# Kernel optimization log

Hardware: AMD Instinct MI355X
Metric: run time of the kernel (lower is better)

The kernel has to match this reference:

```python
import jax, jax.numpy as jnp
import numpy as np

LN_EPS = 1e-5


def setup_inputs() -> dict:
    key = jax.random.key(0)
    ks = jax.random.split(key, 10)
    B, T, D, K = 32, 1024, 512, 3
    enc = jax.random.normal(ks[0], (B, T, D), jnp.float32)
    dur = jax.random.randint(ks[1], (B, T), 0, 7, jnp.int32)
    s = 0.02
    return {
        "encoder_output": enc,
        "duration_target": dur,
        "conv1_w": jax.random.normal(ks[2], (K, D, D), jnp.float32) * s,  # HIO layout
        "conv1_b": jnp.zeros((D,), jnp.float32),
        "ln1_w": jnp.ones((D,), jnp.float32),
        "ln1_b": jnp.zeros((D,), jnp.float32),
        "conv2_w": jax.random.normal(ks[3], (K, D, D), jnp.float32) * s,
        "conv2_b": jnp.zeros((D,), jnp.float32),
        "ln2_w": jnp.ones((D,), jnp.float32),
        "ln2_b": jnp.zeros((D,), jnp.float32),
        "lin_w": jax.random.normal(ks[4], (D, 1), jnp.float32) * s,
        "lin_b": jnp.zeros((1,), jnp.float32),
        "max_len": 4096,
    }


def _conv_relu(x, w, b):
    # x: [B,T,D], w: [K, D_in, D_out] ('HIO'), 'SAME' padding == torch padding=1 for k=3
    y = jax.lax.conv_general_dilated(
        x, w, window_strides=(1,), padding="SAME",
        dimension_numbers=("NHC", "HIO", "NHC"))
    return jax.nn.relu(y + b)


def _layernorm(x, g, b):
    mu = jnp.mean(x, axis=-1, keepdims=True)
    var = jnp.mean(jnp.square(x - mu), axis=-1, keepdims=True)
    return (x - mu) * jax.lax.rsqrt(var + LN_EPS) * g + b


def reference(encoder_output, duration_target, conv1_w, conv1_b, ln1_w, ln1_b,
              conv2_w, conv2_b, ln2_w, ln2_b, lin_w, lin_b, max_len):
    B, T, D = encoder_output.shape
    # duration predictor: conv -> relu -> LN -> conv -> relu -> LN -> linear
    h = _layernorm(_conv_relu(encoder_output, conv1_w, conv1_b), ln1_w, ln1_b)
    h = _layernorm(_conv_relu(h, conv2_w, conv2_b), ln2_w, ln2_b)
    duration_predictor_output = (h @ lin_w + lin_b)[..., 0]  # [B,T]

    # training path: expand by duration_target via fused gather with cumulative offsets
    cum = jnp.cumsum(duration_target, axis=1)          # [B,T]
    pos = jnp.arange(max_len, dtype=jnp.int32)         # [L]
    # src index for output frame j: first t with cum[t] > j
    idx = jax.vmap(lambda c: jnp.searchsorted(c, pos, side="right"))(cum)  # [B,L]
    valid = pos[None, :] < cum[:, -1:]                  # [B,L]
    idx = jnp.minimum(idx, T - 1)
    expanded = jnp.take_along_axis(encoder_output, idx[:, :, None], axis=1)
    expanded = expanded * valid[:, :, None].astype(encoder_output.dtype)
    return expanded, duration_predictor_output
```

## Files before the change

kernel.cpp:

```cpp
#include <hip/hip_runtime.h>
#include <hip/hip_bf16.h>

#define BB 32
#define TT 1024
#define DD 512
#define LL 4096
#define KDIM 1536
#define TP 1026
#define ROWS (BB * TT)
#define NT (KDIM / 32)

typedef __attribute__((ext_vector_type(8))) short short8;
typedef __attribute__((ext_vector_type(8))) unsigned short ushort8;
typedef __attribute__((ext_vector_type(4))) float floatx4;

__device__ __forceinline__ unsigned short f2bf(float f) {
  unsigned int u = __builtin_bit_cast(unsigned int, f);
  u += 0x7FFF + ((u >> 16) & 1);
  return (unsigned short)(u >> 16);
}
__device__ __forceinline__ float bf2f(unsigned short h) {
  return __builtin_bit_cast(float, (unsigned int)h << 16);
}

#define GLOAD_LDS16(g, l)                                          \
  __builtin_amdgcn_global_load_lds(                                \
      (const __attribute__((address_space(1))) void*)(g),          \
      (__attribute__((address_space(3))) void*)(l), 16, 0, 0)

#define PAD_BLKS ((BB * TP) / 4)
#define W0 (PAD_BLKS + 16)
#define C0 (W0 + 384)
#define PREP_BLKS (C0 + 32)

__global__ __launch_bounds__(256) void prep_kernel(
    const float* __restrict__ X, unsigned short* __restrict__ Xp,
    unsigned short* __restrict__ Hp,
    const float* __restrict__ W1, unsigned short* __restrict__ Wt1,
    const float* __restrict__ W2, unsigned short* __restrict__ Wt2,
    const int* __restrict__ dur, int* __restrict__ cum) {
  __shared__ float tile[64][65];
  const int tid = threadIdx.x;
  const int lane = tid & 63;

  if (blockIdx.x >= C0) {
    int* ls = reinterpret_cast<int*>(tile);
    const int b = blockIdx.x - C0;
    int4 v = reinterpret_cast<const int4*>(dur + b * TT)[tid];
    const int s0 = v.x, s1 = s0 + v.y, s2 = s1 + v.z, s3 = s2 + v.w;
    ls[tid] = s3;
    __syncthreads();
    for (int off = 1; off < 256; off <<= 1) {
      int x = (tid >= off) ? ls[tid - off] : 0;
      __syncthreads();
      ls[tid] += x;
      __syncthreads();
    }
    const int base = tid ? ls[tid - 1] : 0;
    int4 o = {base + s0, base + s1, base + s2, base + s3};
    reinterpret_cast<int4*>(cum + b * TT)[tid] = o;
    return;
  }
  if (blockIdx.x >= W0) {
    const int w = blockIdx.x - W0;
    const int z = w / 192;
    const int rem = w - z * 192;
    const int bx = rem & 7;
    const int by = rem >> 3;
    const float* W = z ? W2 : W1;
    unsigned short* Wt = z ? Wt2 : Wt1;
    const int n0 = bx * 64;
    const int k0 = by * 64;
    const int c = lane;
    const int r4 = tid >> 6;
#pragma unroll
    for (int r = 0; r < 16; ++r)
      tile[r * 4 + r4][c] = W[(long)(k0 + r * 4 + r4) * DD + n0 + c];
    __syncthreads();
#pragma unroll
    for (int r = 0; r < 16; ++r)
      Wt[(long)(n0 + r * 4 + r4) * KDIM + k0 + c] = f2bf(tile[c][r * 4 + r4]);
    return;
  }
  if (blockIdx.x >= PAD_BLKS) {
    const int hid = (blockIdx.x - PAD_BLKS) * 4 + (tid >> 6);
    const int b = hid >> 1;
    const long r = (long)b * TP + ((hid & 1) ? (TP - 1) : 0);
    *reinterpret_cast<ushort8*>(Hp + r * DD + lane * 8) = (ushort8)0;
    return;
  }
  const int row = blockIdx.x * 4 + (tid >> 6);
  const int b  = row / TP;
  const int pr = row - b * TP;
  ushort8* o = reinterpret_cast<ushort8*>(Xp + (long)row * DD + lane * 8);
  ushort8 v;
  if (pr == 0 || pr == TP - 1) {
    v = (ushort8)0;
  } else {
    const float* p = X + ((long)(b * TT + pr - 1)) * DD + lane * 8;
    float4 a = *reinterpret_cast<const float4*>(p);
    float4 c = *reinterpret_cast<const float4*>(p + 4);
    v[0] = f2bf(a.x); v[1] = f2bf(a.y); v[2] = f2bf(a.z); v[3] = f2bf(a.w);
    v[4] = f2bf(c.x); v[5] = f2bf(c.y); v[6] = f2bf(c.z); v[7] = f2bf(c.w);
  }
  *o = v;
}

template <int LAYER>
__global__ __launch_bounds__(512, 2) void fused_conv_ln_kernel(
    const unsigned short* __restrict__ Xp, const unsigned short* __restrict__ Wt,
    const float* __restrict__ bias, const float* __restrict__ g,
    const float* __restrict__ be, const float* __restrict__ lw,
    const float* __restrict__ lb, unsigned short* __restrict__ Hp,
    float* __restrict__ dpo) {
  __shared__ unsigned short As[3][128 * 32];
  __shared__ unsigned short Bs[3][512 * 32];
  __shared__ float sS[4][128];
  __shared__ float sQ[4][128];
  __shared__ float muL[128];
  __shared__ float rsL[128];

  const int tid  = threadIdx.x;
  const int lane = tid & 63;
  const int wid  = tid >> 6;
  const int srow = lane >> 2;
  const int gchunk = (lane & 3) ^ (srow & 3);
  const int frow = lane & 15;
  const int quad = lane >> 4;
  const int rdch = quad ^ (frow & 3);
  const int wm = (wid >> 2) * 64;
  const int wn = (wid & 3) * 128;
  const int wc = wid & 3;

  const int m0 = blockIdx.x * 128;
  const int bA = m0 >> 10;
  const int t0 = m0 & (TT - 1);

  const unsigned short* gA0 =
      Xp + (long)(bA * TP + t0 + wid * 16 + srow) * DD + gchunk * 8;
  const unsigned short* gB0 =
      Wt + (long)(wid * 16 + srow) * KDIM + gchunk * 8;

  floatx4 acc[4][8];
#pragma unroll
  for (int i = 0; i < 4; ++i)
#pragma unroll
    for (int j = 0; j < 8; ++j) acc[i][j] = (floatx4){0.f, 0.f, 0.f, 0.f};

#define STAGE(bi, kk)                                                         \
  do {                                                                        \
    const int tap_ = (kk) >> 9;                                               \
    const int c0_  = (kk) & 511;                                              \
    GLOAD_LDS16(gA0 + (long)tap_ * DD + c0_, &As[bi][(wid * 16) * 32]);       \
    GLOAD_LDS16(gB0 + (kk),                   &Bs[bi][(wid * 16) * 32]);      \
    GLOAD_LDS16(gB0 + (long)128 * KDIM + (kk), &Bs[bi][(128 + wid * 16) * 32]); \
    GLOAD_LDS16(gB0 + (long)256 * KDIM + (kk), &Bs[bi][(256 + wid * 16) * 32]); \
    GLOAD_LDS16(gB0 + (long)384 * KDIM + (kk), &Bs[bi][(384 + wid * 16) * 32]); \
  } while (0)

#define COMPUTE(bi)                                                           \
  do {                                                                        \
    short8 a_[4], b_[8];                                                      \
    _Pragma("unroll")                                                         \
    for (int i = 0; i < 4; ++i)                                               \
      a_[i] = *reinterpret_cast<const short8*>(                               \
          &As[bi][(wm + i * 16 + frow) * 32 + rdch * 8]);                     \
    _Pragma("unroll")                                                         \
    for (int j = 0; j < 8; ++j)                                               \
      b_[j] = *reinterpret_cast<const short8*>(                               \
          &Bs[bi][(wn + j * 16 + frow) * 32 + rdch * 8]);                     \
    _Pragma("unroll")                                                         \
    for (int i = 0; i < 4; ++i)                                               \
      _Pragma("unroll")                                                       \
      for (int j = 0; j < 8; ++j)                                             \
        acc[i][j] = __builtin_amdgcn_mfma_f32_16x16x32_bf16(                  \
            a_[i], b_[j], acc[i][j], 0, 0, 0);                                \
  } while (0)

  STAGE(0, 0);
  STAGE(1, 32);

  int cur = 0;
  int stg = 2;
  for (int t = 0; t < NT - 1; ++t) {
    asm volatile("s_waitcnt vmcnt(5)" ::: "memory");
    __builtin_amdgcn_s_barrier();
    __builtin_amdgcn_sched_barrier(0);
    if (t + 2 < NT) STAGE(stg, (t + 2) * 32);
    COMPUTE(cur);
    cur = (cur == 2) ? 0 : cur + 1;
    stg = (stg == 2) ? 0 : stg + 1;
  }
  asm volatile("s_waitcnt vmcnt(0)" ::: "memory");
  __builtin_amdgcn_s_barrier();
  __builtin_amdgcn_sched_barrier(0);
  COMPUTE(cur);
#undef STAGE
#undef COMPUTE

  float bz[8];
#pragma unroll
  for (int j = 0; j < 8; ++j) bz[j] = bias[wn + j * 16 + frow];
#pragma unroll
  for (int i = 0; i < 4; ++i)
#pragma unroll
    for (int j = 0; j < 8; ++j)
#pragma unroll
      for (int r = 0; r < 4; ++r)
        acc[i][j][r] = fmaxf(acc[i][j][r] + bz[j], 0.f);

  float ps[16], pq[16];
#pragma unroll
  for (int i = 0; i < 4; ++i)
#pragma unroll
    for (int r = 0; r < 4; ++r) {
      float s = 0.f, q = 0.f;
#pragma unroll
      for (int j = 0; j < 8; ++j) {
        const float v = acc[i][j][r];
        s += v; q += v * v;
      }
      ps[i * 4 + r] = s; pq[i * 4 + r] = q;
    }
#pragma unroll
  for (int off = 1; off < 16; off <<= 1)
#pragma unroll
    for (int k = 0; k < 16; ++k) {
      ps[k] += __shfl_xor(ps[k], off);
      pq[k] += __shfl_xor(pq[k], off);
    }
  if (frow == 0) {
#pragma unroll
    for (int i = 0; i < 4; ++i)
#pragma unroll
      for (int r = 0; r < 4; ++r) {
        const int row = wm + i * 16 + quad * 4 + r;
        sS[wc][row] = ps[i * 4 + r];
        sQ[wc][row] = pq[i * 4 + r];
      }
  }
  __syncthreads();
  if (tid < 128) {
    const float s = sS[0][tid] + sS[1][tid] + sS[2][tid] + sS[3][tid];
    const float q = sQ[0][tid] + sQ[1][tid] + sQ[2][tid] + sQ[3][tid];
    const float mu = s * (1.f / DD);
    const float var = q * (1.f / DD) - mu * mu;
    muL[tid] = mu;
    rsL[tid] = rsqrtf(var + 1e-5f);
  }
  __syncthreads();

  float gg[8], bb[8];
#pragma unroll
  for (int j = 0; j < 8; ++j) {
    gg[j] = g[wn + j * 16 + frow];
    bb[j] = be[wn + j * 16 + frow];
  }

  if constexpr (LAYER == 1) {
    unsigned short* Ls = &Bs[0][0];
    const int h = wm >> 6;
#pragma unroll
    for (int ph = 0; ph < 2; ++ph) {
      __syncthreads();
      if (h == ph) {
#pragma unroll
        for (int i = 0; i < 4; ++i)
#pragma unroll
          for (int r = 0; r < 4; ++r) {
            const int row = wm + i * 16 + quad * 4 + r;
            const float mu = muL[row];
            const float rs = rsL[row];
            const int lrow = row - ph * 64;
#pragma unroll
            for (int j = 0; j < 8; ++j) {
              const float v = (acc[i][j][r] - mu) * rs * gg[j] + bb[j];
              Ls[lrow * 520 + wn + j * 16 + frow] = f2bf(v);
            }
          }
      }
      __syncthreads();
      const long gbase = (long)(bA * TP + t0 + ph * 64 + 1) * DD;
#pragma unroll
      for (int it = 0; it < 8; ++it) {
        const int r2 = it * 8 + wid;
        const int cc = lane * 8;
        ushort8 val = *reinterpret_cast<const ushort8*>(&Ls[r2 * 520 + cc]);
        *reinterpret_cast<ushort8*>(&Hp[gbase + (long)r2 * DD + cc]) = val;
      }
    }
  } else {
    float ww[8];
#pragma unroll
    for (int j = 0; j < 8; ++j) ww[j] = lw[wn + j * 16 + frow];
#pragma unroll
    for (int i = 0; i < 4; ++i)
#pragma unroll
      for (int r = 0; r < 4; ++r) {
        const int row = wm + i * 16 + quad * 4 + r;
        const float mu = muL[row];
        const float rs = rsL[row];
        float d = 0.f;
#pragma unroll
        for (int j = 0; j < 8; ++j) {
          const float v = (acc[i][j][r] - mu) * rs * gg[j] + bb[j];
          d += v * ww[j];
        }
#pragma unroll
        for (int off = 1; off < 16; off <<= 1) d += __shfl_xor(d, off);
        if (frow == 0) sS[wc][row] = d;
      }
    __syncthreads();
    if (tid < 128)
      dpo[m0 + tid] =
          sS[0][tid] + sS[1][tid] + sS[2][tid] + sS[3][tid] + lb[0];
  }
}

__global__ __launch_bounds__(512) void gather_kernel(
    const float* __restrict__ X, const int* __restrict__ cum,
    float* __restrict__ out) {
  const long gf = (long)blockIdx.x * 4 + (threadIdx.x >> 7);
  const int tl = threadIdx.x & 127;
  const int b = (int)(gf >> 12);
  const int j = (int)(gf & (LL - 1));
  const int* c = cum + b * TT;
  floatx4* o = reinterpret_cast<floatx4*>(out + gf * DD) + tl;
  const int total = c[TT - 1];
  if (j >= total) {
    __builtin_nontemporal_store((floatx4){0.f, 0.f, 0.f, 0.f}, o);
    return;
  }
  int lo = 0, hi = TT - 1;
  while (lo < hi) {
    const int mid = (lo + hi) >> 1;
    if (c[mid] <= j) lo = mid + 1; else hi = mid;
  }
  const floatx4* src =
      reinterpret_cast<const floatx4*>(X + ((long)b * TT + lo) * DD) + tl;
  __builtin_nontemporal_store(*src, o);
}

extern "C" void kernel_launch(void* const* d_in, const int* in_sizes, int n_in,
                              void* d_out, int out_size, void* d_ws,
                              size_t ws_size, hipStream_t stream) {
  const float* enc = (const float*)d_in[0];
  const int* dur   = (const int*)d_in[1];
  const float* w1  = (const float*)d_in[2];
  const float* b1  = (const float*)d_in[3];
  const float* g1  = (const float*)d_in[4];
  const float* be1 = (const float*)d_in[5];
  const float* w2  = (const float*)d_in[6];
  const float* b2  = (const float*)d_in[7];
  const float* g2  = (const float*)d_in[8];
  const float* be2 = (const float*)d_in[9];
  const float* lw  = (const float*)d_in[10];
  const float* lb  = (const float*)d_in[11];

  float* out = (float*)d_out;
  float* expanded = out;
  float* dpo = out + (long)BB * LL * DD;

  unsigned short* enc_pad = (unsigned short*)(expanded);
  unsigned short* h1_pad  = (unsigned short*)(expanded + 9000000);
  unsigned short* wt1     = (unsigned short*)(expanded + 18000000);
  unsigned short* wt2     = (unsigned short*)(expanded + 18400000);
  int* cum = (int*)d_ws;

  prep_kernel<<<PREP_BLKS, 256, 0, stream>>>(enc, enc_pad, h1_pad, w1, wt1,
                                             w2, wt2, dur, cum);

  fused_conv_ln_kernel<1><<<ROWS / 128, 512, 0, stream>>>(
      enc_pad, wt1, b1, g1, be1, nullptr, nullptr, h1_pad, nullptr);
  fused_conv_ln_kernel<2><<<ROWS / 128, 512, 0, stream>>>(
      h1_pad, wt2, b2, g2, be2, lw, lb, nullptr, dpo);

  gather_kernel<<<BB * LL / 4, 512, 0, stream>>>(enc, cum, expanded);
}
```

Measured before the change: 542.4 us.

## Use 1024-thread conv blocks, precompute gather indices, drop nontemporal stores

The fused conv+LayerNorm kernel now runs 16 waves per block, each owning a 64x64 output tile instead of 64x128. This halves the accumulator registers per wave and raises the number of waves per CU. Source frame indices are now written once in prep_kernel from the cumulative durations, replacing a per-frame binary search in the gather kernel. The gather's nontemporal stores become plain stores. Risks: more LDS traffic per MFMA from the smaller warp tiles, a serial per-thread fill loop in prep, and the 4-blocks-per-CU launch bound may not fit the shared-memory footprint.

```diff
diff --git a/kernel.cpp b/kernel.cpp
--- a/kernel.cpp
+++ b/kernel.cpp
@@ -19,9 +19,6 @@
   u += 0x7FFF + ((u >> 16) & 1);
   return (unsigned short)(u >> 16);
 }
-__device__ __forceinline__ float bf2f(unsigned short h) {
-  return __builtin_bit_cast(float, (unsigned int)h << 16);
-}
 
 #define GLOAD_LDS16(g, l)                                          \
   __builtin_amdgcn_global_load_lds(                                \
@@ -38,7 +35,8 @@
     unsigned short* __restrict__ Hp,
     const float* __restrict__ W1, unsigned short* __restrict__ Wt1,
     const float* __restrict__ W2, unsigned short* __restrict__ Wt2,
-    const int* __restrict__ dur, int* __restrict__ cum) {
+    const int* __restrict__ dur, int* __restrict__ cum,
+    int* __restrict__ idx) {
   __shared__ float tile[64][65];
   const int tid = threadIdx.x;
   const int lane = tid & 63;
@@ -59,6 +57,15 @@
     const int base = tid ? ls[tid - 1] : 0;
     int4 o = {base + s0, base + s1, base + s2, base + s3};
     reinterpret_cast<int4*>(cum + b * TT)[tid] = o;
+    int* ib = idx + b * LL;
+    int st = base;
+    const int dv[4] = {v.x, v.y, v.z, v.w};
+#pragma unroll
+    for (int k = 0; k < 4; ++k) {
+      const int e = min(st + dv[k], LL);
+      for (int j = st; j < e; ++j) ib[j] = 4 * tid + k;
+      st += dv[k];
+    }
     return;
   }
   if (blockIdx.x >= W0) {
@@ -107,7 +114,7 @@
 }
 
 template <int LAYER>
-__global__ __launch_bounds__(512, 2) void fused_conv_ln_kernel(
+__global__ __launch_bounds__(1024, 4) void fused_conv_ln_kernel(
     const unsigned short* __restrict__ Xp, const unsigned short* __restrict__ Wt,
     const float* __restrict__ bias, const float* __restrict__ g,
     const float* __restrict__ be, const float* __restrict__ lw,
@@ -115,8 +122,8 @@
     float* __restrict__ dpo) {
   __shared__ unsigned short As[3][128 * 32];
   __shared__ unsigned short Bs[3][512 * 32];
-  __shared__ float sS[4][128];
-  __shared__ float sQ[4][128];
+  __shared__ float sS[8][128];
+  __shared__ float sQ[8][128];
   __shared__ float muL[128];
   __shared__ float rsL[128];
 
@@ -128,51 +135,51 @@
   const int frow = lane & 15;
   const int quad = lane >> 4;
   const int rdch = quad ^ (frow & 3);
-  const int wm = (wid >> 2) * 64;
-  const int wn = (wid & 3) * 128;
-  const int wc = wid & 3;
+  const int wm = (wid >> 3) * 64;
+  const int wn = (wid & 7) * 64;
+  const int wc = wid & 7;
 
   const int m0 = blockIdx.x * 128;
   const int bA = m0 >> 10;
   const int t0 = m0 & (TT - 1);
 
   const unsigned short* gA0 =
-      Xp + (long)(bA * TP + t0 + wid * 16 + srow) * DD + gchunk * 8;
+      Xp + (long)(bA * TP + t0 + (wid & 7) * 16 + srow) * DD + gchunk * 8;
+  const int bb0 = (wid < 8) ? wid * 32 : 256 + (wid - 8) * 32;
   const unsigned short* gB0 =
-      Wt + (long)(wid * 16 + srow) * KDIM + gchunk * 8;
-
-  floatx4 acc[4][8];
+      Wt + (long)(bb0 + srow) * KDIM + gchunk * 8;
+
+  floatx4 acc[4][4];
 #pragma unroll
   for (int i = 0; i < 4; ++i)
 #pragma unroll
-    for (int j = 0; j < 8; ++j) acc[i][j] = (floatx4){0.f, 0.f, 0.f, 0.f};
+    for (int j = 0; j < 4; ++j) acc[i][j] = (floatx4){0.f, 0.f, 0.f, 0.f};
 
 #define STAGE(bi, kk)                                                         \
   do {                                                                        \
     const int tap_ = (kk) >> 9;                                               \
     const int c0_  = (kk) & 511;                                              \
-    GLOAD_LDS16(gA0 + (long)tap_ * DD + c0_, &As[bi][(wid * 16) * 32]);       \
-    GLOAD_LDS16(gB0 + (kk),                   &Bs[bi][(wid * 16) * 32]);      \
-    GLOAD_LDS16(gB0 + (long)128 * KDIM + (kk), &Bs[bi][(128 + wid * 16) * 32]); \
-    GLOAD_LDS16(gB0 + (long)256 * KDIM + (kk), &Bs[bi][(256 + wid * 16) * 32]); \
-    GLOAD_LDS16(gB0 + (long)384 * KDIM + (kk), &Bs[bi][(384 + wid * 16) * 32]); \
+    if (wid < 8)                                                              \
+      GLOAD_LDS16(gA0 + (long)tap_ * DD + c0_, &As[bi][(wid * 16) * 32]);     \
+    GLOAD_LDS16(gB0 + (kk),                &Bs[bi][bb0 * 32]);                \
+    GLOAD_LDS16(gB0 + (long)16 * KDIM + (kk), &Bs[bi][(bb0 + 16) * 32]);      \
   } while (0)
 
 #define COMPUTE(bi)                                                           \
   do {                                                                        \
-    short8 a_[4], b_[8];                                                      \
+    short8 a_[4], b_[4];                                                      \
     _Pragma("unroll")                                                         \
     for (int i = 0; i < 4; ++i)                                               \
       a_[i] = *reinterpret_cast<const short8*>(                               \
           &As[bi][(wm + i * 16 + frow) * 32 + rdch * 8]);                     \
     _Pragma("unroll")                                                         \
-    for (int j = 0; j < 8; ++j)                                               \
+    for (int j = 0; j < 4; ++j)                                               \
       b_[j] = *reinterpret_cast<const short8*>(                               \
           &Bs[bi][(wn + j * 16 + frow) * 32 + rdch * 8]);                     \
     _Pragma("unroll")                                                         \
     for (int i = 0; i < 4; ++i)                                               \
       _Pragma("unroll")                                                       \
-      for (int j = 0; j < 8; ++j)                                             \
+      for (int j = 0; j < 4; ++j)                                             \
         acc[i][j] = __builtin_amdgcn_mfma_f32_16x16x32_bf16(                  \
             a_[i], b_[j], acc[i][j], 0, 0, 0);                                \
   } while (0)
@@ -183,7 +190,8 @@
   int cur = 0;
   int stg = 2;
   for (int t = 0; t < NT - 1; ++t) {
-    asm volatile("s_waitcnt vmcnt(5)" ::: "memory");
+    if (wid < 8) asm volatile("s_waitcnt vmcnt(3)" ::: "memory");
+    else         asm volatile("s_waitcnt vmcnt(2)" ::: "memory");
     __builtin_amdgcn_s_barrier();
     __builtin_amdgcn_sched_barrier(0);
     if (t + 2 < NT) STAGE(stg, (t + 2) * 32);
@@ -198,13 +206,13 @@
 #undef STAGE
 #undef COMPUTE
 
-  float bz[8];
-#pragma unroll
-  for (int j = 0; j < 8; ++j) bz[j] = bias[wn + j * 16 + frow];
+  float bz[4];
+#pragma unroll
+  for (int j = 0; j < 4; ++j) bz[j] = bias[wn + j * 16 + frow];
 #pragma unroll
   for (int i = 0; i < 4; ++i)
 #pragma unroll
-    for (int j = 0; j < 8; ++j)
+    for (int j = 0; j < 4; ++j)
 #pragma unroll
       for (int r = 0; r < 4; ++r)
         acc[i][j][r] = fmaxf(acc[i][j][r] + bz[j], 0.f);
@@ -216,7 +224,7 @@
     for (int r = 0; r < 4; ++r) {
       float s = 0.f, q = 0.f;
 #pragma unroll
-      for (int j = 0; j < 8; ++j) {
+      for (int j = 0; j < 4; ++j) {
         const float v = acc[i][j][r];
         s += v; q += v * v;
       }
@@ -241,8 +249,9 @@
   }
   __syncthreads();
   if (tid < 128) {
-    const float s = sS[0][tid] + sS[1][tid] + sS[2][tid] + sS[3][tid];
-    const float q = sQ[0][tid] + sQ[1][tid] + sQ[2][tid] + sQ[3][tid];
+    float s = 0.f, q = 0.f;
+#pragma unroll
+    for (int c = 0; c < 8; ++c) { s += sS[c][tid]; q += sQ[c][tid]; }
     const float mu = s * (1.f / DD);
     const float var = q * (1.f / DD) - mu * mu;
     muL[tid] = mu;
@@ -250,9 +259,9 @@
   }
   __syncthreads();
 
-  float gg[8], bb[8];
-#pragma unroll
-  for (int j = 0; j < 8; ++j) {
+  float gg[4], bb[4];
+#pragma unroll
+  for (int j = 0; j < 4; ++j) {
     gg[j] = g[wn + j * 16 + frow];
     bb[j] = be[wn + j * 16 + frow];
   }
@@ -273,7 +282,7 @@
             const float rs = rsL[row];
             const int lrow = row - ph * 64;
 #pragma unroll
-            for (int j = 0; j < 8; ++j) {
+            for (int j = 0; j < 4; ++j) {
               const float v = (acc[i][j][r] - mu) * rs * gg[j] + bb[j];
               Ls[lrow * 520 + wn + j * 16 + frow] = f2bf(v);
             }
@@ -282,17 +291,17 @@
       __syncthreads();
       const long gbase = (long)(bA * TP + t0 + ph * 64 + 1) * DD;
 #pragma unroll
-      for (int it = 0; it < 8; ++it) {
-        const int r2 = it * 8 + wid;
+      for (int it = 0; it < 4; ++it) {
+        const int r2 = it * 16 + wid;
         const int cc = lane * 8;
         ushort8 val = *reinterpret_cast<const ushort8*>(&Ls[r2 * 520 + cc]);
         *reinterpret_cast<ushort8*>(&Hp[gbase + (long)r2 * DD + cc]) = val;
       }
     }
   } else {
-    float ww[8];
-#pragma unroll
-    for (int j = 0; j < 8; ++j) ww[j] = lw[wn + j * 16 + frow];
+    float ww[4];
+#pragma unroll
+    for (int j = 0; j < 4; ++j) ww[j] = lw[wn + j * 16 + frow];
 #pragma unroll
     for (int i = 0; i < 4; ++i)
 #pragma unroll
@@ -302,7 +311,7 @@
         const float rs = rsL[row];
         float d = 0.f;
 #pragma unroll
-        for (int j = 0; j < 8; ++j) {
+        for (int j = 0; j < 4; ++j) {
           const float v = (acc[i][j][r] - mu) * rs * gg[j] + bb[j];
           d += v * ww[j];
         }
@@ -311,34 +320,32 @@
         if (frow == 0) sS[wc][row] = d;
       }
     __syncthreads();
-    if (tid < 128)
-      dpo[m0 + tid] =
-          sS[0][tid] + sS[1][tid] + sS[2][tid] + sS[3][tid] + lb[0];
+    if (tid < 128) {
+      float s = lb[0];
+#pragma unroll
+      for (int c = 0; c < 8; ++c) s += sS[c][tid];
+      dpo[blockIdx.x * 128 + tid] = s;
+    }
   }
 }
 
 __global__ __launch_bounds__(512) void gather_kernel(
     const float* __restrict__ X, const int* __restrict__ cum,
-    float* __restrict__ out) {
+    const int* __restrict__ idx, float* __restrict__ out) {
   const long gf = (long)blockIdx.x * 4 + (threadIdx.x >> 7);
   const int tl = threadIdx.x & 127;
   const int b = (int)(gf >> 12);
   const int j = (int)(gf & (LL - 1));
-  const int* c = cum + b * TT;
+  const int total = cum[b * TT + TT - 1];
   floatx4* o = reinterpret_cast<floatx4*>(out + gf * DD) + tl;
-  const int total = c[TT - 1];
   if (j >= total) {
-    __builtin_nontemporal_store((floatx4){0.f, 0.f, 0.f, 0.f}, o);
+    *o = (floatx4){0.f, 0.f, 0.f, 0.f};
     return;
   }
-  int lo = 0, hi = TT - 1;
-  while (lo < hi) {
-    const int mid = (lo + hi) >> 1;
-    if (c[mid] <= j) lo = mid + 1; else hi = mid;
-  }
+  const int lo = idx[b * LL + j];
   const floatx4* src =
       reinterpret_cast<const floatx4*>(X + ((long)b * TT + lo) * DD) + tl;
-  __builtin_nontemporal_store(*src, o);
+  *o = *src;
 }
 
 extern "C" void kernel_launch(void* const* d_in, const int* in_sizes, int n_in,
@@ -366,14 +373,15 @@
   unsigned short* wt1     = (unsigned short*)(expanded + 18000000);
   unsigned short* wt2     = (unsigned short*)(expanded + 18400000);
   int* cum = (int*)d_ws;
+  int* idx = (int*)d_ws + ROWS;
 
   prep_kernel<<<PREP_BLKS, 256, 0, stream>>>(enc, enc_pad, h1_pad, w1, wt1,
-                                             w2, wt2, dur, cum);
-
-  fused_conv_ln_kernel<1><<<ROWS / 128, 512, 0, stream>>>(
+                                             w2, wt2, dur, cum, idx);
+
+  fused_conv_ln_kernel<1><<<ROWS / 128, 1024, 0, stream>>>(
       enc_pad, wt1, b1, g1, be1, nullptr, nullptr, h1_pad, nullptr);
-  fused_conv_ln_kernel<2><<<ROWS / 128, 512, 0, stream>>>(
+  fused_conv_ln_kernel<2><<<ROWS / 128, 1024, 0, stream>>>(
       h1_pad, wt2, b2, g2, be2, lw, lb, nullptr, dpo);
 
-  gather_kernel<<<BB * LL / 4, 512, 0, stream>>>(enc, cum, expanded);
-}
+  gather_kernel<<<BB * LL / 4, 512, 0, stream>>>(enc, cum, idx, expanded);
+}
```

Measured after the change: 513.7 us. 5.3% less time.

## Split MFMA step into halves, widen LDS swizzle, precompute gather indices

Applied to the files above, without the earlier changes.

The GEMM main loop now loads B fragments in two halves. Each half is followed by an explicit lgkmcnt wait, and the MFMA blocks run at raised priority with a barrier between them, which interleaves LDS reads with matrix math. The LDS XOR swizzle gains an extra term to reduce bank conflicts. The prep kernel now writes a per-frame source index table, so the gather kernel replaces its per-thread binary search with one lookup. The gather also switches from nontemporal stores to plain stores. Building the index table with serial per-thread loops adds some prep time and workspace use.

```diff
diff --git a/kernel.cpp b/kernel.cpp
--- a/kernel.cpp
+++ b/kernel.cpp
@@ -19,9 +19,6 @@
   u += 0x7FFF + ((u >> 16) & 1);
   return (unsigned short)(u >> 16);
 }
-__device__ __forceinline__ float bf2f(unsigned short h) {
-  return __builtin_bit_cast(float, (unsigned int)h << 16);
-}
 
 #define GLOAD_LDS16(g, l)                                          \
   __builtin_amdgcn_global_load_lds(                                \
@@ -38,7 +35,8 @@
     unsigned short* __restrict__ Hp,
     const float* __restrict__ W1, unsigned short* __restrict__ Wt1,
     const float* __restrict__ W2, unsigned short* __restrict__ Wt2,
-    const int* __restrict__ dur, int* __restrict__ cum) {
+    const int* __restrict__ dur, int* __restrict__ cum,
+    int* __restrict__ idx) {
   __shared__ float tile[64][65];
   const int tid = threadIdx.x;
   const int lane = tid & 63;
@@ -59,6 +57,15 @@
     const int base = tid ? ls[tid - 1] : 0;
     int4 o = {base + s0, base + s1, base + s2, base + s3};
     reinterpret_cast<int4*>(cum + b * TT)[tid] = o;
+    int* ib = idx + b * LL;
+    int st = base;
+    const int dv[4] = {v.x, v.y, v.z, v.w};
+#pragma unroll
+    for (int k = 0; k < 4; ++k) {
+      const int e = min(st + dv[k], LL);
+      for (int j = st; j < e; ++j) ib[j] = 4 * tid + k;
+      st += dv[k];
+    }
     return;
   }
   if (blockIdx.x >= W0) {
@@ -124,10 +131,10 @@
   const int lane = tid & 63;
   const int wid  = tid >> 6;
   const int srow = lane >> 2;
-  const int gchunk = (lane & 3) ^ (srow & 3);
+  const int gchunk = (lane & 3) ^ (srow & 3) ^ ((srow >> 2) & 3);
   const int frow = lane & 15;
   const int quad = lane >> 4;
-  const int rdch = quad ^ (frow & 3);
+  const int rdch = quad ^ (frow & 3) ^ ((frow >> 2) & 3);
   const int wm = (wid >> 2) * 64;
   const int wn = (wid & 3) * 128;
   const int wc = wid & 3;
@@ -158,23 +165,45 @@
     GLOAD_LDS16(gB0 + (long)384 * KDIM + (kk), &Bs[bi][(384 + wid * 16) * 32]); \
   } while (0)
 
-#define COMPUTE(bi)                                                           \
+#define STEP(bi, do_stage, stage_bi, stage_kk)                                \
   do {                                                                        \
+    __builtin_amdgcn_sched_barrier(0);                                        \
+    if (do_stage) STAGE(stage_bi, stage_kk);                                  \
     short8 a_[4], b_[8];                                                      \
     _Pragma("unroll")                                                         \
     for (int i = 0; i < 4; ++i)                                               \
       a_[i] = *reinterpret_cast<const short8*>(                               \
           &As[bi][(wm + i * 16 + frow) * 32 + rdch * 8]);                     \
     _Pragma("unroll")                                                         \
-    for (int j = 0; j < 8; ++j)                                               \
+    for (int j = 0; j < 4; ++j)                                               \
       b_[j] = *reinterpret_cast<const short8*>(                               \
           &Bs[bi][(wn + j * 16 + frow) * 32 + rdch * 8]);                     \
+    asm volatile("s_waitcnt lgkmcnt(0)" ::: "memory");                        \
+    __builtin_amdgcn_sched_barrier(0);                                        \
+    __builtin_amdgcn_s_setprio(1);                                            \
     _Pragma("unroll")                                                         \
     for (int i = 0; i < 4; ++i)                                               \
       _Pragma("unroll")                                                       \
-      for (int j = 0; j < 8; ++j)                                             \
+      for (int j = 0; j < 4; ++j)                                             \
         acc[i][j] = __builtin_amdgcn_mfma_f32_16x16x32_bf16(                  \
             a_[i], b_[j], acc[i][j], 0, 0, 0);                                \
+    __builtin_amdgcn_s_setprio(0);                                            \
+    __builtin_amdgcn_s_barrier();                                             \
+    __builtin_amdgcn_sched_barrier(0);                                        \
+    _Pragma("unroll")                                                         \
+    for (int j = 0; j < 4; ++j)                                               \
+      b_[4 + j] = *reinterpret_cast<const short8*>(                           \
+          &Bs[bi][(wn + 64 + j * 16 + frow) * 32 + rdch * 8]);                \
+    asm volatile("s_waitcnt lgkmcnt(0)" ::: "memory");                        \
+    __builtin_amdgcn_sched_barrier(0);                                        \
+    __builtin_amdgcn_s_setprio(1);                                            \
+    _Pragma("unroll")                                                         \
+    for (int i = 0; i < 4; ++i)                                               \
+      _Pragma("unroll")                                                       \
+      for (int j = 0; j < 4; ++j)                                             \
+        acc[i][4 + j] = __builtin_amdgcn_mfma_f32_16x16x32_bf16(              \
+            a_[i], b_[4 + j], acc[i][4 + j], 0, 0, 0);                        \
+    __builtin_amdgcn_s_setprio(0);                                            \
   } while (0)
 
   STAGE(0, 0);
@@ -185,18 +214,15 @@
   for (int t = 0; t < NT - 1; ++t) {
     asm volatile("s_waitcnt vmcnt(5)" ::: "memory");
     __builtin_amdgcn_s_barrier();
-    __builtin_amdgcn_sched_barrier(0);
-    if (t + 2 < NT) STAGE(stg, (t + 2) * 32);
-    COMPUTE(cur);
+    STEP(cur, (t + 2 < NT), stg, (t + 2) * 32);
     cur = (cur == 2) ? 0 : cur + 1;
     stg = (stg == 2) ? 0 : stg + 1;
   }
   asm volatile("s_waitcnt vmcnt(0)" ::: "memory");
   __builtin_amdgcn_s_barrier();
-  __builtin_amdgcn_sched_barrier(0);
-  COMPUTE(cur);
+  STEP(cur, false, 0, 0);
+#undef STEP
 #undef STAGE
-#undef COMPUTE
 
   float bz[8];
 #pragma unroll
@@ -312,33 +338,28 @@
       }
     __syncthreads();
     if (tid < 128)
-      dpo[m0 + tid] =
+      dpo[blockIdx.x * 128 + tid] =
           sS[0][tid] + sS[1][tid] + sS[2][tid] + sS[3][tid] + lb[0];
   }
 }
 
 __global__ __launch_bounds__(512) void gather_kernel(
     const float* __restrict__ X, const int* __restrict__ cum,
-    float* __restrict__ out) {
+    const int* __restrict__ idx, float* __restrict__ out) {
   const long gf = (long)blockIdx.x * 4 + (threadIdx.x >> 7);
   const int tl = threadIdx.x & 127;
   const int b = (int)(gf >> 12);
   const int j = (int)(gf & (LL - 1));
-  const int* c = cum + b * TT;
+  const int total = cum[b * TT + TT - 1];
   floatx4* o = reinterpret_cast<floatx4*>(out + gf * DD) + tl;
-  const int total = c[TT - 1];
   if (j >= total) {
-    __builtin_nontemporal_store((floatx4){0.f, 0.f, 0.f, 0.f}, o);
+    *o = (floatx4){0.f, 0.f, 0.f, 0.f};
     return;
   }
-  int lo = 0, hi = TT - 1;
-  while (lo < hi) {
-    const int mid = (lo + hi) >> 1;
-    if (c[mid] <= j) lo = mid + 1; else hi = mid;
-  }
+  const int lo = idx[b * LL + j];
   const floatx4* src =
       reinterpret_cast<const floatx4*>(X + ((long)b * TT + lo) * DD) + tl;
-  __builtin_nontemporal_store(*src, o);
+  *o = *src;
 }
 
 extern "C" void kernel_launch(void* const* d_in, const int* in_sizes, int n_in,
@@ -366,14 +387,15 @@
   unsigned short* wt1     = (unsigned short*)(expanded + 18000000);
   unsigned short* wt2     = (unsigned short*)(expanded + 18400000);
   int* cum = (int*)d_ws;
+  int* idx = (int*)d_ws + ROWS;
 
   prep_kernel<<<PREP_BLKS, 256, 0, stream>>>(enc, enc_pad, h1_pad, w1, wt1,
-                                             w2, wt2, dur, cum);
+                                             w2, wt2, dur, cum, idx);
 
   fused_conv_ln_kernel<1><<<ROWS / 128, 512, 0, stream>>>(
       enc_pad, wt1, b1, g1, be1, nullptr, nullptr, h1_pad, nullptr);
   fused_conv_ln_kernel<2><<<ROWS / 128, 512, 0, stream>>>(
       h1_pad, wt2, b2, g2, be2, lw, lb, nullptr, dpo);
 
-  gather_kernel<<<BB * LL / 4, 512, 0, stream>>>(enc, cum, expanded);
+  gather_kernel<<<BB * LL / 4, 512, 0, stream>>>(enc, cum, idx, expanded);
 }
```

New measurement: 518.7 us. -4.4%, faster.
